# Performance work log

Measured on AMD Instinct MI355X. Metric: run time of the kernel, lower is better.

Reference implementation:

```python
import jax, jax.numpy as jnp
import numpy as np

H = 32        # query heads
KVH = 8       # key/value heads
D = 64        # head_dim
HID = 2048
B, S = 2, 2048

def rotate_half(x):
    x1, x2 = x[..., :D // 2], x[..., D // 2:]
    return jnp.concatenate((-x2, x1), axis=-1)

def setup_inputs() -> dict:
    key = jax.random.key(0)
    ks = jax.random.split(key, 7)
    scale = 1.0 / np.sqrt(HID)
    return {
        "x": jax.random.normal(ks[0], (B, S, HID), jnp.float32),
        "cos": jax.random.uniform(ks[1], (S, D), jnp.float32),
        "sin": jax.random.uniform(ks[2], (S, D), jnp.float32),
        "wq": jax.random.normal(ks[3], (HID, H * D), jnp.float32) * scale,
        "wk": jax.random.normal(ks[4], (HID, KVH * D), jnp.float32) * scale,
        "wv": jax.random.normal(ks[5], (HID, KVH * D), jnp.float32) * scale,
        "wo": jax.random.normal(ks[6], (HID, HID), jnp.float32) * scale,
    }

def reference(x, cos, sin, wq, wk, wv, wo):
    b, s, _ = x.shape
    # QKV projections -> [b, heads, s, d]
    q = (x @ wq).reshape(b, s, H, D).transpose(0, 2, 1, 3)
    k = (x @ wk).reshape(b, s, KVH, D).transpose(0, 2, 1, 3)
    v = (x @ wv).reshape(b, s, KVH, D).transpose(0, 2, 1, 3)
    # RoPE (cos/sin broadcast over batch and heads)
    c = cos[None, None, :, :]
    si = sin[None, None, :, :]
    q = q * c + rotate_half(q) * si
    k = k * c + rotate_half(k) * si
    # GQA: expand kv heads (repeat_interleave on head axis)
    g = H // KVH
    k = jnp.repeat(k, g, axis=1)
    v = jnp.repeat(v, g, axis=1)
    # causal SDPA
    scores = jnp.einsum("bhqd,bhkd->bhqk", q, k) / np.sqrt(D).astype(np.float32)
    causal = jnp.tril(jnp.ones((s, s), dtype=bool))
    scores = jnp.where(causal[None, None], scores, jnp.finfo(scores.dtype).min)
    attn = jax.nn.softmax(scores, axis=-1)
    out = jnp.einsum("bhqk,bhkd->bhqd", attn, v)
    out = out.transpose(0, 2, 1, 3).reshape(b, s, H * D)
    return out @ wo
```

## Files before the change

kernel.cpp:

```cpp
#include <hip/hip_runtime.h>
#include <stdint.h>

#define B_ 2
#define S_ 2048
#define H_ 32
#define KVH_ 8
#define D_ 64
#define HID_ 2048

typedef float f32x4 __attribute__((ext_vector_type(4)));
typedef float f32x16 __attribute__((ext_vector_type(16)));
typedef short bf16x8 __attribute__((ext_vector_type(8)));
typedef unsigned short u16;
typedef unsigned short u16x4 __attribute__((ext_vector_type(4)));
typedef unsigned short u16x8 __attribute__((ext_vector_type(8)));
typedef unsigned int u32;
typedef unsigned int u32x2 __attribute__((ext_vector_type(2)));
typedef unsigned int u32x4 __attribute__((ext_vector_type(4)));

__device__ __forceinline__ u16 f2b(float f) {
  unsigned u = __builtin_bit_cast(unsigned, f);
  u += 0x7fffu + ((u >> 16) & 1u);
  return (u16)(u >> 16);
}
__device__ __forceinline__ float b2f(u16 h) {
  unsigned u = ((unsigned)h) << 16;
  return __builtin_bit_cast(float, u);
}
__device__ __forceinline__ void gl_lds16(const void* g, void* l) {
  __builtin_amdgcn_global_load_lds(
      (const __attribute__((address_space(1))) unsigned*)g,
      (__attribute__((address_space(3))) unsigned*)l, 16, 0, 0);
}
__device__ __forceinline__ f32x4 mfma16(bf16x8 a, bf16x8 b, f32x4 c) {
  return __builtin_amdgcn_mfma_f32_16x16x32_bf16(a, b, c, 0, 0, 0);
}
__device__ __forceinline__ f32x16 mfma32(bf16x8 a, bf16x8 b, f32x16 c) {
  return __builtin_amdgcn_mfma_f32_32x32x16_bf16(a, b, c, 0, 0, 0);
}
__device__ __forceinline__ u32 cvtpk(float lo, float hi) {
  u32 r;
  asm("v_cvt_pk_bf16_f32 %0, %1, %2" : "=v"(r) : "v"(lo), "v"(hi));
  return r;
}
__device__ __forceinline__ float fast_exp2(float x) {
#if __has_builtin(__builtin_amdgcn_exp2f)
  return __builtin_amdgcn_exp2f(x);
#else
  return exp2f(x);
#endif
}
__device__ __forceinline__ void swap32(u32 a, u32 b, u32& x, u32& y) {
#if __has_builtin(__builtin_amdgcn_permlane32_swap)
  auto r = __builtin_amdgcn_permlane32_swap(a, b, false, false);
  x = r[0];
  y = r[1];
#else
  u32 sa = (u32)__shfl_xor((int)a, 32), sb = (u32)__shfl_xor((int)b, 32);
  bool hib = (threadIdx.x & 32) != 0;
  x = hib ? sb : a;
  y = hib ? b : sa;
#endif
}

__global__ __launch_bounds__(256) void k_cvt(const float* __restrict__ src,
                                             u16* __restrict__ dst, int n4) {
  int i = blockIdx.x * 256 + threadIdx.x;
  if (i >= n4) return;
  f32x4 v = *(const f32x4*)(src + (size_t)i * 4);
  u16x4 o;
  o[0] = f2b(v[0]); o[1] = f2b(v[1]); o[2] = f2b(v[2]); o[3] = f2b(v[3]);
  *(u16x4*)(dst + (size_t)i * 4) = o;
}

__global__ __launch_bounds__(256) void k_transpose(const float* __restrict__ src,
                                                   u16* __restrict__ dst,
                                                   int K, int N) {
  __shared__ float t[32][33];
  int n0 = blockIdx.x * 32, k0 = blockIdx.y * 32;
  int tt = threadIdx.x;
  int r = tt >> 3, c4 = (tt & 7) << 2;
  f32x4 v = *(const f32x4*)(src + (size_t)(k0 + r) * N + n0 + c4);
  t[r][c4 + 0] = v[0]; t[r][c4 + 1] = v[1];
  t[r][c4 + 2] = v[2]; t[r][c4 + 3] = v[3];
  __syncthreads();
  u16x4 o;
  o[0] = f2b(t[c4 + 0][r]); o[1] = f2b(t[c4 + 1][r]);
  o[2] = f2b(t[c4 + 2][r]); o[3] = f2b(t[c4 + 3][r]);
  *(u16x4*)(dst + (size_t)(n0 + r) * K + k0 + c4) = o;
}

__device__ __forceinline__ void stage64(const u16* __restrict__ G, int rowbase,
                                        int K, int kt, u16* unit, int tid) {
  int r = tid >> 3, sl = tid & 7;
  gl_lds16(G + (size_t)(rowbase + r) * K + kt * 64 + ((sl ^ (r & 7)) << 3),
           (char*)unit + tid * 16);
}

template <int BN, int OUTF32>
__global__ __launch_bounds__(512, 1) void k_gemm8(const u16* __restrict__ A,
                                                  const u16* __restrict__ BT,
                                                  float* __restrict__ Cf,
                                                  u16* __restrict__ Cb,
                                                  int M, int N, int K) {
  constexpr int ATILE = 256 * 64;
  constexpr int BTILE = BN * 64;
  constexpr int BU = BN / 64;
  constexpr int WN = (BN == 128) ? 2 : 4;
  constexpr int NI = (BN == 192) ? 3 : 4;
  constexpr int MI = (BN == 128) ? 4 : 8;
  constexpr int MIP = MI / 4;
  __shared__ __align__(16) u16 sm[2 * ATILE + 2 * BTILE];
  const int tid = threadIdx.x;
  const int l = tid & 63;
  const int lg = (l >> 4) & 3, lr = l & 15;
  const int w = tid >> 6;
  const int wm = w / WN, wn = w % WN;

  const int nwg = gridDim.x;
  const int cpx = nwg >> 3;
  const int bid = blockIdx.x;
  const int swz = (bid & 7) * cpx + (bid >> 3);
  const int ntn = N / BN;
  const int bm = swz / ntn, bn = swz % ntn;
  const int m0 = bm << 8, n0 = bn * BN;

  const u16* Ag = A + (size_t)m0 * K;
  const u16* Bg = BT + (size_t)n0 * K;
  u16* As = sm;
  u16* Bs = sm + 2 * ATILE;

  const int nt = K >> 6;
  f32x4 acc[MI][NI] = {};

#pragma unroll
  for (int u = 0; u < 4; ++u) stage64(Ag, u * 64, K, 0, As + u * 4096, tid);
#pragma unroll
  for (int u = 0; u < BU; ++u) stage64(Bg, u * 64, K, 0, Bs + u * 4096, tid);
  stage64(Ag, 0, K, 1, As + ATILE, tid);
  stage64(Ag, 64, K, 1, As + ATILE + 4096, tid);
  asm volatile("s_waitcnt vmcnt(2)" ::: "memory");
  __builtin_amdgcn_s_barrier();
  asm volatile("" ::: "memory");

  for (int t = 0; t < nt; ++t) {
    const int cur = t & 1;
    u16* Ac = As + cur * ATILE;
    u16* Bc = Bs + cur * BTILE;
    u16* An = As + (cur ^ 1) * ATILE;
    u16* Bn = Bs + (cur ^ 1) * BTILE;
    bf16x8 bc[NI][2];
#pragma unroll
    for (int q = 0; q < 4; ++q) {
      bf16x8 af[MIP][2];
#pragma unroll
      for (int mi2 = 0; mi2 < MIP; ++mi2)
#pragma unroll
        for (int ks = 0; ks < 2; ++ks) {
          int row = wm * (MI * 16) + (q * MIP + mi2) * 16 + lr;
          int slot = (ks * 4 + lg) ^ (lr & 7);
          af[mi2][ks] = *(const bf16x8*)&Ac[row * 64 + slot * 8];
        }
      if (q == 0) {
#pragma unroll
        for (int ni = 0; ni < NI; ++ni)
#pragma unroll
          for (int ks = 0; ks < 2; ++ks) {
            int row = wn * (NI * 16) + ni * 16 + lr;
            int slot = (ks * 4 + lg) ^ (lr & 7);
            bc[ni][ks] = *(const bf16x8*)&Bc[row * 64 + slot * 8];
          }
      }
      if (t + 1 < nt) {
        if (q == 0) {
          stage64(Ag, 128, K, t + 1, An + 2 * 4096, tid);
          stage64(Ag, 192, K, t + 1, An + 3 * 4096, tid);
        } else if (q == 1) {
          stage64(Bg, 0, K, t + 1, Bn, tid);
          stage64(Bg, 64, K, t + 1, Bn + 4096, tid);
        } else if (q == 2) {
          if (BU >= 3) stage64(Bg, 128, K, t + 1, Bn + 2 * 4096, tid);
          if (BU >= 4) stage64(Bg, 192, K, t + 1, Bn + 3 * 4096, tid);
        }
      }
      __builtin_amdgcn_s_barrier();
      asm volatile("" ::: "memory");
      __builtin_amdgcn_s_setprio(1);
#pragma unroll
      for (int mi2 = 0; mi2 < MIP; ++mi2)
#pragma unroll
        for (int ni = 0; ni < NI; ++ni)
#pragma unroll
          for (int ks = 0; ks < 2; ++ks)
            acc[q * MIP + mi2][ni] =
                mfma16(af[mi2][ks], bc[ni][ks], acc[q * MIP + mi2][ni]);
      __builtin_amdgcn_s_setprio(0);
      if (q == 3) {
        if (t + 2 < nt) {
          stage64(Ag, 0, K, t + 2, Ac, tid);
          stage64(Ag, 64, K, t + 2, Ac + 4096, tid);
          asm volatile("s_waitcnt vmcnt(2)" ::: "memory");
        } else if (t + 1 < nt) {
          asm volatile("s_waitcnt vmcnt(0)" ::: "memory");
        }
      }
      __builtin_amdgcn_s_barrier();
      asm volatile("" ::: "memory");
    }
  }

#pragma unroll
  for (int mi = 0; mi < MI; ++mi)
#pragma unroll
    for (int ni = 0; ni < NI; ++ni)
#pragma unroll
      for (int j = 0; j < 4; ++j) {
        size_t row = (size_t)m0 + wm * (MI * 16) + mi * 16 + lg * 4 + j;
        size_t col = (size_t)n0 + wn * (NI * 16) + ni * 16 + lr;
        if (OUTF32)
          Cf[row * N + col] = acc[mi][ni][j];
        else
          Cb[row * N + col] = f2b(acc[mi][ni][j]);
      }
}

__global__ __launch_bounds__(256) void k_rope(const u16* __restrict__ qkv,
                                              const float* __restrict__ cosb,
                                              const float* __restrict__ sinb,
                                              u16* __restrict__ Qr,
                                              u16* __restrict__ Kr) {
  int task = blockIdx.x * 16 + (threadIdx.x >> 4);
  int t16 = threadIdx.x & 15;
  int head = task % (H_ + KVH_);
  int row = task / (H_ + KVH_);
  int b = row >> 11, s = row & (S_ - 1);
  int d2 = t16 * 2;
  const u16* base =
      qkv + (size_t)row * 3072 + (head < H_ ? head * 64 : 2048 + (head - H_) * 64);
  u32 lo = *(const u32*)(base + d2);
  u32 hi = *(const u32*)(base + d2 + 32);
  float xl0 = b2f((u16)lo), xl1 = b2f((u16)(lo >> 16));
  float xh0 = b2f((u16)hi), xh1 = b2f((u16)(hi >> 16));
  const float* cb = cosb + s * 64;
  const float* sb = sinb + s * 64;
  float cl0 = cb[d2], cl1 = cb[d2 + 1], ch0 = cb[d2 + 32], ch1 = cb[d2 + 33];
  float sl0 = sb[d2], sl1 = sb[d2 + 1], sh0 = sb[d2 + 32], sh1 = sb[d2 + 33];
  float sc = (head < H_) ? 0.18033688f : 1.0f;
  float ol0 = (xl0 * cl0 - xh0 * sl0) * sc;
  float ol1 = (xl1 * cl1 - xh1 * sl1) * sc;
  float oh0 = (xh0 * ch0 + xl0 * sh0) * sc;
  float oh1 = (xh1 * ch1 + xl1 * sh1) * sc;
  u16* dst = (head < H_)
                 ? Qr + ((size_t)(b * H_ + head) * S_ + s) * 64
                 : Kr + ((size_t)(b * KVH_ + (head - H_)) * S_ + s) * 64;
  *(u32*)(dst + d2) = (u32)f2b(ol0) | ((u32)f2b(ol1) << 16);
  *(u32*)(dst + d2 + 32) = (u32)f2b(oh0) | ((u32)f2b(oh1) << 16);
}

__global__ __launch_bounds__(256) void k_vtrans(const u16* __restrict__ qkv,
                                                u16* __restrict__ Vt) {
  int bid = blockIdx.x;
  int st = bid & 31, kvh = (bid >> 5) & 7, b = bid >> 8;
  int s0 = st * 64;
  __shared__ u16 t[64][72];
  int tid = threadIdx.x;
  int sl = tid >> 2, c16 = (tid & 3) << 4;
  const u16* src = qkv + (size_t)(b * S_ + s0 + sl) * 3072 + 2560 + kvh * 64 + c16;
  u16x8 v0 = *(const u16x8*)src;
  u16x8 v1 = *(const u16x8*)(src + 8);
#pragma unroll
  for (int i = 0; i < 8; ++i) { t[sl][c16 + i] = v0[i]; t[sl][c16 + 8 + i] = v1[i]; }
  __syncthreads();
  int dl = tid >> 2, s16 = (tid & 3) << 4;
  u16x8 o0, o1;
#pragma unroll
  for (int i = 0; i < 8; ++i) { o0[i] = t[s16 + i][dl]; o1[i] = t[s16 + 8 + i][dl]; }
  u16* dst = Vt + ((size_t)(b * KVH_ + kvh) * 64 + dl) * S_ + s0 + s16;
  *(u16x8*)dst = o0;
  *(u16x8*)(dst + 8) = o1;
}

__device__ __forceinline__ void stage_kv8(const u16* __restrict__ Kg,
                                          const u16* __restrict__ Vg, int k0,
                                          u16* ldsK, u16* ldsV, int tid) {
  int r = tid >> 3, cc = tid & 7;
  gl_lds16(Kg + (size_t)(k0 + r) * 64 + ((cc ^ (r & 7)) << 3), ldsK + tid * 8);
  gl_lds16(Vg + (size_t)r * S_ + k0 + ((cc ^ (r & 7)) << 3), ldsV + tid * 8);
}

__device__ __forceinline__ void repack2(const f32x16 s, bf16x8& f0, bf16x8& f1) {
  bf16x8 outv[2];
#pragma unroll
  for (int h = 0; h < 2; ++h) {
    u32 a0 = cvtpk(s[8 * h + 0], s[8 * h + 1]);
    u32 a1 = cvtpk(s[8 * h + 4], s[8 * h + 5]);
    u32 b0 = cvtpk(s[8 * h + 2], s[8 * h + 3]);
    u32 b1 = cvtpk(s[8 * h + 6], s[8 * h + 7]);
    u32 x0, y0, x1, y1;
    swap32(a0, a1, x0, y0);
    swap32(b0, b1, x1, y1);
    u32x4 t;
    t[0] = x0; t[1] = x1; t[2] = y0; t[3] = y1;
    outv[h] = __builtin_bit_cast(bf16x8, t);
  }
  f0 = outv[0];
  f1 = outv[1];
}

__global__ __launch_bounds__(512) void k_attn(const u16* __restrict__ Q,
                                              const u16* __restrict__ Kr,
                                              const u16* __restrict__ Vt,
                                              u16* __restrict__ Oout) {
  __shared__ __align__(16) u16 lds[16384];
  const int tid = threadIdx.x;
  const int w = tid >> 6, l = tid & 63;
  const int hi = l >> 5, l31 = l & 31;

  const int bid = blockIdx.x;
  const int qtl = 7 - (bid >> 6);
  const int hh = (bid >> 1) & 31;
  const int b = bid & 1;
  const int kvh = hh >> 2;
  const int q0 = qtl * 256;
  const int qw0 = q0 + w * 32;
  const int nt = 4 * qtl + 4;

  int off8[4];
#pragma unroll
  for (int c = 0; c < 4; ++c)
    off8[c] = l31 * 64 + ((((c << 1) | hi) ^ (l31 & 7)) << 3);

  const size_t qrow = (size_t)((b * H_ + hh) * S_ + qw0 + l31) * 64;
  bf16x8 qf[4];
#pragma unroll
  for (int c = 0; c < 4; ++c)
    qf[c] = *(const bf16x8*)&Q[qrow + c * 16 + hi * 8];

  const u16* Kg = Kr + (size_t)(b * KVH_ + kvh) * S_ * 64;
  const u16* Vg = Vt + (size_t)(b * KVH_ + kvh) * 64 * S_;

  f32x16 o0 = {}, o1 = {};
  float l_run = 0.f;

  stage_kv8(Kg, Vg, 0, lds, lds + 4096, tid);
  asm volatile("s_waitcnt vmcnt(0)" ::: "memory");
  __builtin_amdgcn_s_barrier();
  asm volatile("" ::: "memory");

  for (int kt = 0; kt < nt; ++kt) {
    const int cur = kt & 1;
    const int k0 = kt * 64;
    if (kt + 1 < nt)
      stage_kv8(Kg, Vg, k0 + 64, lds + (cur ^ 1) * 8192,
                lds + (cur ^ 1) * 8192 + 4096, tid);

    if (k0 <= qw0 + 31) {
      const u16* Kc = lds + cur * 8192;
      const u16* Vc = Kc + 4096;

      f32x16 sl = {}, sh = {};
      __builtin_amdgcn_s_setprio(1);
#pragma unroll
      for (int c = 0; c < 4; ++c) {
        bf16x8 klo = *(const bf16x8*)(Kc + off8[c]);
        bf16x8 khi = *(const bf16x8*)(Kc + 2048 + off8[c]);
        sl = mfma32(klo, qf[c], sl);
        sh = mfma32(khi, qf[c], sh);
      }
      __builtin_amdgcn_s_setprio(0);

      if (k0 + 63 > qw0) {
        int qg = qw0 + l31;
#pragma unroll
        for (int r = 0; r < 16; ++r) {
          int kg = k0 + (r & 3) + 8 * (r >> 2) + 4 * hi;
          if (kg > qg) sl[r] = -3e38f;
          if (kg + 32 > qg) sh[r] = -3e38f;
        }
      }

      float smv[16];
#pragma unroll
      for (int i = 0; i < 16; ++i) {
        sl[i] = fast_exp2(sl[i]);
        sh[i] = fast_exp2(sh[i]);
        smv[i] = sl[i] + sh[i];
      }
#pragma unroll
      for (int i = 0; i < 8; ++i) smv[i] += smv[i + 8];
#pragma unroll
      for (int i = 0; i < 4; ++i) smv[i] += smv[i + 4];
      smv[0] = (smv[0] + smv[2]) + (smv[1] + smv[3]);
      l_run += smv[0] + __shfl_xor(smv[0], 32);

      bf16x8 pf[4];
      repack2(sl, pf[0], pf[1]);
      repack2(sh, pf[2], pf[3]);

      __builtin_amdgcn_s_setprio(1);
#pragma unroll
      for (int sub = 0; sub < 4; ++sub) {
        bf16x8 v0 = *(const bf16x8*)(Vc + off8[sub]);
        bf16x8 v1 = *(const bf16x8*)(Vc + 2048 + off8[sub]);
        o0 = mfma32(v0, pf[sub], o0);
        o1 = mfma32(v1, pf[sub], o1);
      }
      __builtin_amdgcn_s_setprio(0);
    }

    asm volatile("s_waitcnt vmcnt(0)" ::: "memory");
    __builtin_amdgcn_s_barrier();
    asm volatile("" ::: "memory");
  }

  {
    u16* ep = lds + w * 2048;
    float inv = 1.0f / l_run;
    float oc[32];
#pragma unroll
    for (int i = 0; i < 16; ++i) { oc[i] = o0[i]; oc[16 + i] = o1[i]; }
#pragma unroll
    for (int dh = 0; dh < 2; ++dh)
#pragma unroll
      for (int g = 0; g < 4; ++g) {
        u32 w0 = cvtpk(oc[dh * 16 + 4 * g + 0] * inv, oc[dh * 16 + 4 * g + 1] * inv);
        u32 w1 = cvtpk(oc[dh * 16 + 4 * g + 2] * inv, oc[dh * 16 + 4 * g + 3] * inv);
        int col = dh * 32 + 8 * g + 4 * hi;
        u32x2 tw; tw[0] = w0; tw[1] = w1;
        *(u32x2*)&ep[l31 * 64 + col] = tw;
      }
    asm volatile("s_waitcnt lgkmcnt(0)" ::: "memory");
    int row = l >> 1;
    size_t gb = ((size_t)(b * S_ + q0 + w * 32 + row)) * HID_ + hh * 64 + (l & 1) * 32;
#pragma unroll
    for (int cc = 0; cc < 4; ++cc) {
      u16x8 v = *(const u16x8*)&ep[row * 64 + (l & 1) * 32 + cc * 8];
      *(u16x8*)&Oout[gb + cc * 8] = v;
    }
  }
}

extern "C" void kernel_launch(void* const* d_in, const int* in_sizes, int n_in,
                              void* d_out, int out_size, void* d_ws, size_t ws_size,
                              hipStream_t stream) {
  (void)in_sizes; (void)n_in; (void)out_size; (void)ws_size;
  const float* x    = (const float*)d_in[0];
  const float* cosb = (const float*)d_in[1];
  const float* sinb = (const float*)d_in[2];
  const float* wq   = (const float*)d_in[3];
  const float* wk   = (const float*)d_in[4];
  const float* wv   = (const float*)d_in[5];
  const float* wo   = (const float*)d_in[6];

  char* wsb = (char*)d_ws;
  u16* xb    = (u16*)(wsb + 0);
  u16* wqkvT = (u16*)(wsb + 16777216);
  u16* woT   = (u16*)(wsb + 29360128);
  u16* qkv   = (u16*)(wsb + 37748736);
  u16* attno = qkv;
  u16* Qr    = (u16*)(wsb + 62914560);
  u16* Kr    = (u16*)(wsb + 79691776);
  u16* Vt    = (u16*)(wsb + 83886080);

  k_cvt<<<8192, 256, 0, stream>>>(x, xb, (B_ * S_ * HID_) / 4);
  k_transpose<<<dim3(64, 64), 256, 0, stream>>>(wq, wqkvT, 2048, 2048);
  k_transpose<<<dim3(16, 64), 256, 0, stream>>>(wk, wqkvT + (size_t)2048 * 2048, 2048, 512);
  k_transpose<<<dim3(16, 64), 256, 0, stream>>>(wv, wqkvT + (size_t)2560 * 2048, 2048, 512);
  k_transpose<<<dim3(64, 64), 256, 0, stream>>>(wo, woT, 2048, 2048);

  k_gemm8<192, 0><<<256, 512, 0, stream>>>(xb, wqkvT, nullptr, qkv, 4096, 3072, 2048);

  k_rope<<<10240, 256, 0, stream>>>(qkv, cosb, sinb, Qr, Kr);
  k_vtrans<<<512, 256, 0, stream>>>(qkv, Vt);

  k_attn<<<512, 512, 0, stream>>>(Qr, Kr, Vt, attno);

  k_gemm8<128, 1><<<256, 512, 0, stream>>>(attno, woT, (float*)d_out, nullptr,
                                           4096, 2048, 2048);
}
```

Baseline: 185.1 us.

## Triple-buffer B tiles in GEMM and prefetch them two iterations ahead

The bf16 GEMM kernel now keeps three LDS buffers for the B operand instead of two and issues B loads two k-tiles ahead. A tiles stay double-buffered, but each whole A tile is now loaded in one burst at the start of the iteration rather than split across sub-steps. The prologue preloads A0, A1, B0, B1 and B2, and the vmcnt waits are rewritten for the new load counts. The goal is to hide more global-load latency for B. The cost is more LDS (which may use nearly all of it at BN=256) and burstier A traffic with a shorter prefetch distance for A.

```diff
diff --git a/kernel.cpp b/kernel.cpp
--- a/kernel.cpp
+++ b/kernel.cpp
@@ -110,7 +110,7 @@
   constexpr int NI = (BN == 192) ? 3 : 4;
   constexpr int MI = (BN == 128) ? 4 : 8;
   constexpr int MIP = MI / 4;
-  __shared__ __align__(16) u16 sm[2 * ATILE + 2 * BTILE];
+  __shared__ __align__(16) u16 sm[2 * ATILE + 3 * BTILE];
   const int tid = threadIdx.x;
   const int l = tid & 63;
   const int lg = (l >> 4) & 3, lr = l & 15;
@@ -137,18 +137,24 @@
   for (int u = 0; u < 4; ++u) stage64(Ag, u * 64, K, 0, As + u * 4096, tid);
 #pragma unroll
   for (int u = 0; u < BU; ++u) stage64(Bg, u * 64, K, 0, Bs + u * 4096, tid);
-  stage64(Ag, 0, K, 1, As + ATILE, tid);
-  stage64(Ag, 64, K, 1, As + ATILE + 4096, tid);
-  asm volatile("s_waitcnt vmcnt(2)" ::: "memory");
+#pragma unroll
+  for (int u = 0; u < 4; ++u) stage64(Ag, u * 64, K, 1, As + ATILE + u * 4096, tid);
+#pragma unroll
+  for (int u = 0; u < BU; ++u)
+    stage64(Bg, u * 64, K, 1, Bs + BTILE + u * 4096, tid);
+#pragma unroll
+  for (int u = 0; u < BU; ++u)
+    stage64(Bg, u * 64, K, 2, Bs + 2 * BTILE + u * 4096, tid);
+  if constexpr (BU == 3)
+    asm volatile("s_waitcnt vmcnt(10)" ::: "memory");
+  else
+    asm volatile("s_waitcnt vmcnt(8)" ::: "memory");
   __builtin_amdgcn_s_barrier();
   asm volatile("" ::: "memory");
 
   for (int t = 0; t < nt; ++t) {
-    const int cur = t & 1;
-    u16* Ac = As + cur * ATILE;
-    u16* Bc = Bs + cur * BTILE;
-    u16* An = As + (cur ^ 1) * ATILE;
-    u16* Bn = Bs + (cur ^ 1) * BTILE;
+    u16* Ac = As + (t & 1) * ATILE;
+    u16* Bc = Bs + (t % 3) * BTILE;
     bf16x8 bc[NI][2];
 #pragma unroll
     for (int q = 0; q < 4; ++q) {
@@ -170,17 +176,19 @@
             int slot = (ks * 4 + lg) ^ (lr & 7);
             bc[ni][ks] = *(const bf16x8*)&Bc[row * 64 + slot * 8];
           }
-      }
-      if (t + 1 < nt) {
-        if (q == 0) {
-          stage64(Ag, 128, K, t + 1, An + 2 * 4096, tid);
-          stage64(Ag, 192, K, t + 1, An + 3 * 4096, tid);
-        } else if (q == 1) {
-          stage64(Bg, 0, K, t + 1, Bn, tid);
-          stage64(Bg, 64, K, t + 1, Bn + 4096, tid);
-        } else if (q == 2) {
-          if (BU >= 3) stage64(Bg, 128, K, t + 1, Bn + 2 * 4096, tid);
-          if (BU >= 4) stage64(Bg, 192, K, t + 1, Bn + 3 * 4096, tid);
+        if (t >= 1) {
+          if (t + 1 < nt) {
+            u16* An = As + ((t + 1) & 1) * ATILE;
+#pragma unroll
+            for (int u = 0; u < 4; ++u)
+              stage64(Ag, u * 64, K, t + 1, An + u * 4096, tid);
+          }
+          if (t + 2 < nt) {
+            u16* Bn = Bs + ((t + 2) % 3) * BTILE;
+#pragma unroll
+            for (int u = 0; u < BU; ++u)
+              stage64(Bg, u * 64, K, t + 2, Bn + u * 4096, tid);
+          }
         }
       }
       __builtin_amdgcn_s_barrier();
@@ -197,9 +205,10 @@
       __builtin_amdgcn_s_setprio(0);
       if (q == 3) {
         if (t + 2 < nt) {
-          stage64(Ag, 0, K, t + 2, Ac, tid);
-          stage64(Ag, 64, K, t + 2, Ac + 4096, tid);
-          asm volatile("s_waitcnt vmcnt(2)" ::: "memory");
+          if constexpr (BU == 3)
+            asm volatile("s_waitcnt vmcnt(3)" ::: "memory");
+          else
+            asm volatile("s_waitcnt vmcnt(2)" ::: "memory");
         } else if (t + 1 < nt) {
           asm volatile("s_waitcnt vmcnt(0)" ::: "memory");
         }
```

Measured after the change: 190.4 us. 2.9% more time.
